# Kernel optimization log

Hardware: AMD Instinct MI355X
Metric: run time of the kernel (lower is better)

## Reference

```python
import jax, jax.numpy as jnp
import numpy as np

N, E, D, H, DH = 10000, 160000, 1024, 4, 256  # nodes, edges, feat dim, heads, per-head dim
NB, G = 3, 64  # num_blocks, num graphs in batch
NEG_SLOPE = 0.2  # PyG GATConv default


def setup_inputs() -> dict:
    key = jax.random.key(0)
    ks = jax.random.split(key, 8)
    x = jax.random.normal(ks[0], (N, D), jnp.float32)
    edge_index = jax.random.randint(ks[1], (2, E), 0, N)
    batch = jnp.sort(jax.random.randint(ks[2], (N,), 0, G))
    W = jax.random.normal(ks[3], (NB, D, H * DH), jnp.float32) * 0.03
    a_src = jax.random.normal(ks[4], (NB, H, DH), jnp.float32) * 0.1
    a_dst = jax.random.normal(ks[5], (NB, H, DH), jnp.float32) * 0.1
    b = jnp.zeros((NB, H * DH), jnp.float32)
    Wr = jax.random.normal(ks[6], (D, 2), jnp.float32) * 0.03
    br = jnp.zeros((2,), jnp.float32)
    return dict(x=x, edge_index=edge_index, batch=batch, W=W, a_src=a_src,
                a_dst=a_dst, b=b, Wr=Wr, br=br)


def _gat_conv(x, src, dst, W, asrc, adst, bias):
    # Linear projection per head: [N, H, DH]
    h = (x @ W).reshape(N, H, DH)
    # Per-node attention logits (src/dst halves of the GAT attention vector)
    es = jnp.einsum('nhd,hd->nh', h, asrc)  # [N, H]
    ed = jnp.einsum('nhd,hd->nh', h, adst)  # [N, H]
    # Edge scores + LeakyReLU
    e = jax.nn.leaky_relu(es[src] + ed[dst], NEG_SLOPE)  # [Etot, H]
    # Segment softmax over edges sharing the same destination node
    m = jax.ops.segment_max(e, dst, num_segments=N)
    p = jnp.exp(e - m[dst])
    s = jax.ops.segment_sum(p, dst, num_segments=N)
    alpha = p / (s[dst] + 1e-16)  # [Etot, H]
    # Scatter-aggregate weighted source features
    out = jax.ops.segment_sum(h[src] * alpha[:, :, None], dst, num_segments=N)
    return out.reshape(N, H * DH) + bias


def reference(x, edge_index, batch, W, a_src, a_dst, b, Wr, br):
    # PyG GATConv adds self-loops by default
    loops = jnp.arange(N)
    src = jnp.concatenate([edge_index[0], loops])
    dst = jnp.concatenate([edge_index[1], loops])
    # Faithful to the source: each block reads the ORIGINAL x; dropout in eval mode.
    h = x
    for i in range(NB):
        h = jax.nn.relu(_gat_conv(x, src, dst, W[i], a_src[i], a_dst[i], b[i]))
    # global_mean_pool over graph assignment `batch`
    sums = jax.ops.segment_sum(h, batch, num_segments=G)
    cnt = jax.ops.segment_sum(jnp.ones((N, 1), h.dtype), batch, num_segments=G)
    pooled = sums / jnp.maximum(cnt, 1.0)
    return pooled @ Wr + br
```

## Files before the change

kernel.cpp:

```cpp
#include <hip/hip_runtime.h>
#include <hip/hip_bf16.h>

#define N_NODES 10000
#define N_EDGES 160000
#define ETOT    (N_NODES + N_EDGES)
#define DIM     1024
#define NHEAD   4
#define DHEAD   256
#define NGRAPH  64
#define NEG_SLOPE 0.2f

typedef short  bf16x8 __attribute__((ext_vector_type(8)));
typedef float  f32x4  __attribute__((ext_vector_type(4)));
typedef unsigned short u16x4 __attribute__((ext_vector_type(4)));
typedef unsigned short u16x8 __attribute__((ext_vector_type(8)));

__device__ __forceinline__ unsigned short f2bf_rne(float v) {
    unsigned u = __builtin_bit_cast(unsigned, v);
    return (unsigned short)((u + 0x7fffu + ((u >> 16) & 1u)) >> 16);
}
__device__ __forceinline__ float bf2f(unsigned short b) {
    return __builtin_bit_cast(float, (unsigned)b << 16);
}
__device__ __forceinline__ float lrelu(float x) { return x > 0.f ? x : NEG_SLOPE * x; }

__global__ __launch_bounds__(256) void prep_x(const float* __restrict__ x,
                                              unsigned short* __restrict__ xhi,
                                              unsigned short* __restrict__ xlo) {
    int i = blockIdx.x * 256 + threadIdx.x;
    if ((size_t)i * 4 >= (size_t)N_NODES * DIM) return;
    f32x4 v = *(const f32x4*)(x + (size_t)i * 4);
    u16x4 hi, lo;
#pragma unroll
    for (int j = 0; j < 4; ++j) {
        unsigned short hb = f2bf_rne(v[j]);
        float r = v[j] - bf2f(hb);
        hi[j] = hb;
        lo[j] = f2bf_rne(r);
    }
    *(u16x4*)(xhi + (size_t)i * 4) = hi;
    *(u16x4*)(xlo + (size_t)i * 4) = lo;
}

__global__ __launch_bounds__(256) void prep_w(const float* __restrict__ W2,
                                              unsigned short* __restrict__ wthi,
                                              unsigned short* __restrict__ wtlo) {
    __shared__ float tile[64][65];
    int bc = blockIdx.x;
    int bk = blockIdx.y;
    int t = threadIdx.x;
    int tj = t & 63, ti = t >> 6;
#pragma unroll
    for (int u = 0; u < 16; ++u) {
        int r = u * 4 + ti;
        tile[r][tj] = W2[(size_t)(bk * 64 + r) * DIM + bc * 64 + tj];
    }
    __syncthreads();
#pragma unroll
    for (int u = 0; u < 16; ++u) {
        int cr = u * 4 + ti;
        float v = tile[tj][cr];
        unsigned short hb = f2bf_rne(v);
        float rres = v - bf2f(hb);
        size_t o = (size_t)(bc * 64 + cr) * DIM + bk * 64 + tj;
        wthi[o] = hb;
        wtlo[o] = f2bf_rne(rres);
    }
}

#define BM 128
#define BN 128
#define BK 32
#define NROWT ((N_NODES + BM - 1) / BM)
#define NCOLT (DIM / BN)

__global__ __launch_bounds__(256) void gemm3(const unsigned short* __restrict__ xhi,
                                             const unsigned short* __restrict__ xlo,
                                             const unsigned short* __restrict__ wthi,
                                             const unsigned short* __restrict__ wtlo,
                                             unsigned short* __restrict__ hb) {
    const int id = blockIdx.x;
    const int xcd = id & 7;
    const int br = xcd + 8 * (id >> 6);
    const int bc = (id >> 3) & 7;
    if (br >= NROWT) return;
    const int r0 = br * BM;
    const int c0 = bc * BN;

    __shared__ short lds[4][BM * BK];
    const int t = threadIdx.x;
    const int lane = t & 63, wid = t >> 6;
    const int wm = wid >> 1, wn = wid & 1;

    const unsigned short* const srcs[4] = {xhi, xlo, wthi, wtlo};
    const unsigned short* wbase = srcs[wid];
    const int rowb = (wid < 2) ? r0 : c0;

    f32x4 acc[4][4];
#pragma unroll
    for (int mi = 0; mi < 4; ++mi)
#pragma unroll
        for (int ni = 0; ni < 4; ++ni) acc[mi][ni] = (f32x4){0.f, 0.f, 0.f, 0.f};

    for (int k0 = 0; k0 < DIM; k0 += BK) {
        __syncthreads();
#pragma unroll
        for (int j = 0; j < 8; ++j) {
            const unsigned short* g = wbase
                + (size_t)(rowb + j * 16 + (lane & 15)) * DIM + k0 + (lane >> 4) * 8;
            __builtin_amdgcn_global_load_lds(
                (const __attribute__((address_space(1))) unsigned int*)g,
                (__attribute__((address_space(3))) unsigned int*)&lds[wid][j * 512],
                16, 0, 0);
        }
        __syncthreads();

        bf16x8 ahi[4], alo[4], bhi[4], blo[4];
#pragma unroll
        for (int mi = 0; mi < 4; ++mi) {
            int sub = wm * 4 + mi;
            ahi[mi] = *(const bf16x8*)&lds[0][sub * 512 + lane * 8];
            alo[mi] = *(const bf16x8*)&lds[1][sub * 512 + lane * 8];
        }
#pragma unroll
        for (int ni = 0; ni < 4; ++ni) {
            int sub = wn * 4 + ni;
            bhi[ni] = *(const bf16x8*)&lds[2][sub * 512 + lane * 8];
            blo[ni] = *(const bf16x8*)&lds[3][sub * 512 + lane * 8];
        }
#pragma unroll
        for (int mi = 0; mi < 4; ++mi)
#pragma unroll
            for (int ni = 0; ni < 4; ++ni) {
                f32x4 c = acc[mi][ni];
                c = __builtin_amdgcn_mfma_f32_16x16x32_bf16(ahi[mi], bhi[ni], c, 0, 0, 0);
                c = __builtin_amdgcn_mfma_f32_16x16x32_bf16(ahi[mi], blo[ni], c, 0, 0, 0);
                c = __builtin_amdgcn_mfma_f32_16x16x32_bf16(alo[mi], bhi[ni], c, 0, 0, 0);
                acc[mi][ni] = c;
            }
    }

#pragma unroll
    for (int mi = 0; mi < 4; ++mi)
#pragma unroll
        for (int ni = 0; ni < 4; ++ni)
#pragma unroll
            for (int v = 0; v < 4; ++v) {
                int row = r0 + wm * 64 + mi * 16 + ((lane >> 4) << 2) + v;
                if (row < N_NODES) {
                    int col = c0 + wn * 64 + ni * 16 + (lane & 15);
                    hb[(size_t)row * DIM + col] = f2bf_rne(acc[mi][ni][v]);
                }
            }
}

__global__ __launch_bounds__(256) void dots_k(const unsigned short* __restrict__ hb,
                                              const float* __restrict__ asrc,
                                              const float* __restrict__ adst,
                                              float* __restrict__ es,
                                              float* __restrict__ ed) {
    int wid = threadIdx.x >> 6, lane = threadIdx.x & 63;
    int n = blockIdx.x * 4 + wid;
    if (n >= N_NODES) return;
    const unsigned short* hr = hb + (size_t)n * DIM + lane * 16;
    u16x8 a = *(const u16x8*)hr;
    u16x8 b8 = *(const u16x8*)(hr + 8);
    const float* ap = asrc + lane * 16;
    const float* dp = adst + lane * 16;
    float sa = 0.f, sd = 0.f;
#pragma unroll
    for (int j = 0; j < 8; ++j) {
        float v = bf2f(a[j]);
        sa += v * ap[j];
        sd += v * dp[j];
    }
#pragma unroll
    for (int j = 0; j < 8; ++j) {
        float v = bf2f(b8[j]);
        sa += v * ap[8 + j];
        sd += v * dp[8 + j];
    }
#pragma unroll
    for (int d = 1; d < 16; d <<= 1) {
        sa += __shfl_xor(sa, d);
        sd += __shfl_xor(sd, d);
    }
    if ((lane & 15) == 0) {
        int head = lane >> 4;
        es[(size_t)n * 4 + head] = sa;
        ed[(size_t)n * 4 + head] = sd;
    }
}

__global__ void init_misc(int* gcnt, int* gbeg, int* gend) {
    int t = threadIdx.x;
    if (t < NGRAPH) { gcnt[t] = 0; gbeg[t] = 0x7fffffff; gend[t] = -1; }
}

__global__ void init_counts(const int* __restrict__ batch, int* cnt, int* cursor,
                            int* gcnt, int* gbeg, int* gend) {
    int n = blockIdx.x * 256 + threadIdx.x;
    if (n >= N_NODES) return;
    cnt[n] = 1;
    cursor[n] = 0;
    int b = batch[n];
    atomicAdd(gcnt + b, 1);
    atomicMin(gbeg + b, n);
    atomicMax(gend + b, n);
}

__global__ void edge_hist(const int* __restrict__ dst, int* cnt) {
    int e = blockIdx.x * 256 + threadIdx.x;
    if (e >= N_EDGES) return;
    atomicAdd(cnt + dst[e], 1);
}

__global__ __launch_bounds__(1024) void scan_k(const int* __restrict__ cnt, int* __restrict__ off) {
    __shared__ int wsh[16];
    __shared__ int tot_s;
    int t = threadIdx.x, lane = t & 63, wv = t >> 6;
    int running = 0;
    for (int c0 = 0; c0 < N_NODES; c0 += 1024) {
        int i = c0 + t;
        int v = (i < N_NODES) ? cnt[i] : 0;
        int s = v;
#pragma unroll
        for (int d = 1; d < 64; d <<= 1) {
            int y = __shfl_up(s, d);
            if (lane >= d) s += y;
        }
        if (lane == 63) wsh[wv] = s;
        __syncthreads();
        if (wv == 0) {
            int wsv = (lane < 16) ? wsh[lane] : 0;
            int e = wsv;
#pragma unroll
            for (int d = 1; d < 16; d <<= 1) {
                int y = __shfl_up(e, d);
                if (lane >= d) e += y;
            }
            if (lane < 16) wsh[lane] = e - wsv;
            if (lane == 15) tot_s = e;
        }
        __syncthreads();
        if (i < N_NODES) off[i] = running + wsh[wv] + s - v;
        running += tot_s;
    }
}

__global__ void bucket_k(const int* __restrict__ src, const int* __restrict__ dst,
                         const int* __restrict__ off, int* cursor, int* bucket) {
    int e = blockIdx.x * 256 + threadIdx.x;
    if (e >= ETOT) return;
    int d = (e < N_EDGES) ? dst[e] : (e - N_EDGES);
    int pos = atomicAdd(cursor + d, 1);
    bucket[off[d] + pos] = e;
}

#define HCAP 192
__global__ __launch_bounds__(256) void aggregate_k(const unsigned short* __restrict__ hb,
                                                   const float* __restrict__ es,
                                                   const float* __restrict__ ed,
                                                   const int* __restrict__ src,
                                                   const int* __restrict__ cnt,
                                                   const int* __restrict__ off,
                                                   const int* __restrict__ bucket,
                                                   const float* __restrict__ b2,
                                                   float* __restrict__ out) {
    int n = blockIdx.x, t = threadIdx.x;
    int deg = cnt[n], base = off[n];
    f32x4 edn = *(const f32x4*)(ed + (size_t)n * 4);
    __shared__ int  s_src[HCAP];
    __shared__ f32x4 s_e[HCAP];
    __shared__ f32x4 wred[4];

    f32x4 m4 = {-3e38f, -3e38f, -3e38f, -3e38f};
    for (int i = t; i < deg; i += 256) {
        int eid = bucket[base + i];
        int s = (eid < N_EDGES) ? src[eid] : (eid - N_EDGES);
        f32x4 e4 = *(const f32x4*)(es + (size_t)s * 4);
        e4.x = lrelu(e4.x + edn.x); e4.y = lrelu(e4.y + edn.y);
        e4.z = lrelu(e4.z + edn.z); e4.w = lrelu(e4.w + edn.w);
        if (i < HCAP) { s_src[i] = s; s_e[i] = e4; }
        m4.x = fmaxf(m4.x, e4.x); m4.y = fmaxf(m4.y, e4.y);
        m4.z = fmaxf(m4.z, e4.z); m4.w = fmaxf(m4.w, e4.w);
    }
#pragma unroll
    for (int d = 1; d < 64; d <<= 1) {
        m4.x = fmaxf(m4.x, __shfl_xor(m4.x, d));
        m4.y = fmaxf(m4.y, __shfl_xor(m4.y, d));
        m4.z = fmaxf(m4.z, __shfl_xor(m4.z, d));
        m4.w = fmaxf(m4.w, __shfl_xor(m4.w, d));
    }
    if ((t & 63) == 0) wred[t >> 6] = m4;
    __syncthreads();
    f32x4 mm = wred[0];
#pragma unroll
    for (int w = 1; w < 4; ++w) {
        mm.x = fmaxf(mm.x, wred[w].x); mm.y = fmaxf(mm.y, wred[w].y);
        mm.z = fmaxf(mm.z, wred[w].z); mm.w = fmaxf(mm.w, wred[w].w);
    }
    int hd = t >> 6;
    float mh = hd == 0 ? mm.x : hd == 1 ? mm.y : hd == 2 ? mm.z : mm.w;

    f32x4 acc = {0.f, 0.f, 0.f, 0.f};
    float sump = 0.f;
    for (int i = 0; i < deg; ++i) {
        int s;
        f32x4 e4;
        if (i < HCAP) { s = s_src[i]; e4 = s_e[i]; }
        else {
            int eid = bucket[base + i];
            s = (eid < N_EDGES) ? src[eid] : (eid - N_EDGES);
            e4 = *(const f32x4*)(es + (size_t)s * 4);
            e4.x = lrelu(e4.x + edn.x); e4.y = lrelu(e4.y + edn.y);
            e4.z = lrelu(e4.z + edn.z); e4.w = lrelu(e4.w + edn.w);
        }
        float eh = hd == 0 ? e4.x : hd == 1 ? e4.y : hd == 2 ? e4.z : e4.w;
        float p = expf(eh - mh);
        sump += p;
        u16x4 q = *(const u16x4*)(hb + (size_t)s * DIM + t * 4);
        f32x4 hv = {bf2f(q[0]), bf2f(q[1]), bf2f(q[2]), bf2f(q[3])};
        acc += p * hv;
    }
    float inv = 1.0f / (sump + 1e-16f);
    f32x4 bb = *(const f32x4*)(b2 + t * 4);
    f32x4 r = acc * inv + bb;
    r.x = fmaxf(r.x, 0.f); r.y = fmaxf(r.y, 0.f);
    r.z = fmaxf(r.z, 0.f); r.w = fmaxf(r.w, 0.f);
    *(f32x4*)(out + (size_t)n * DIM + t * 4) = r;
}

__global__ __launch_bounds__(256) void pool_k(const float* __restrict__ out,
                                              const int* __restrict__ gbeg,
                                              const int* __restrict__ gend,
                                              float* __restrict__ pooled) {
    int g = blockIdx.x, c = blockIdx.y, t = threadIdx.x;
    int col = c * 256 + t;
    int b0 = gbeg[g], b1 = gend[g];
    float acc = 0.f;
    for (int n = b0; n <= b1; ++n) acc += out[(size_t)n * DIM + col];
    pooled[(size_t)g * DIM + col] = acc;
}

__global__ __launch_bounds__(256) void final_k(const float* __restrict__ pooled,
                                               const int* __restrict__ gcnt,
                                               const float* __restrict__ Wr,
                                               const float* __restrict__ br,
                                               float* __restrict__ out) {
    int g = blockIdx.x, t = threadIdx.x;
    float s0 = 0.f, s1 = 0.f;
    for (int d = t; d < DIM; d += 256) {
        float v = pooled[(size_t)g * DIM + d];
        s0 += v * Wr[d * 2];
        s1 += v * Wr[d * 2 + 1];
    }
    __shared__ float r0[256], r1[256];
    r0[t] = s0; r1[t] = s1;
    __syncthreads();
    for (int st = 128; st > 0; st >>= 1) {
        if (t < st) { r0[t] += r0[t + st]; r1[t] += r1[t + st]; }
        __syncthreads();
    }
    if (t == 0) {
        float c = fmaxf((float)gcnt[g], 1.f);
        out[g * 2 + 0] = r0[0] / c + br[0];
        out[g * 2 + 1] = r1[0] / c + br[1];
    }
}

extern "C" void kernel_launch(void* const* d_in, const int* in_sizes, int n_in,
                              void* d_out, int out_size, void* d_ws, size_t ws_size,
                              hipStream_t stream) {
    (void)in_sizes; (void)n_in; (void)out_size; (void)ws_size;
    const float* x     = (const float*)d_in[0];
    const int*   ei    = (const int*)d_in[1];
    const int*   batch = (const int*)d_in[2];
    const float* W     = (const float*)d_in[3];
    const float* a_src = (const float*)d_in[4];
    const float* a_dst = (const float*)d_in[5];
    const float* b     = (const float*)d_in[6];
    const float* Wr    = (const float*)d_in[7];
    const float* br    = (const float*)d_in[8];

    const float* W2    = W + (size_t)2 * DIM * DIM;
    const float* asrc2 = a_src + 2 * NHEAD * DHEAD;
    const float* adst2 = a_dst + 2 * NHEAD * DHEAD;
    const float* b2    = b + 2 * DIM;
    const int* srcI = ei;
    const int* dstI = ei + N_EDGES;

    char* wsp = (char*)d_ws;
    size_t o = 0;
    auto alloc = [&](size_t bytes) -> char* {
        char* p = wsp + o;
        o = (o + bytes + 255) & ~(size_t)255;
        return p;
    };
    unsigned short* xhi  = (unsigned short*)alloc((size_t)N_NODES * DIM * 2);
    unsigned short* xlo  = (unsigned short*)alloc((size_t)N_NODES * DIM * 2);
    unsigned short* wthi = (unsigned short*)alloc((size_t)DIM * DIM * 2);
    unsigned short* wtlo = (unsigned short*)alloc((size_t)DIM * DIM * 2);
    unsigned short* hb   = (unsigned short*)alloc((size_t)N_NODES * DIM * 2);
    float* es   = (float*)alloc((size_t)N_NODES * 4 * 4);
    float* ed   = (float*)alloc((size_t)N_NODES * 4 * 4);
    int*   cnt  = (int*)alloc((size_t)N_NODES * 4);
    int*   offs = (int*)alloc((size_t)N_NODES * 4);
    int*   curs = (int*)alloc((size_t)N_NODES * 4);
    int*   bkt  = (int*)alloc((size_t)ETOT * 4);
    float* pooled = (float*)alloc((size_t)NGRAPH * DIM * 4);
    int*   gcnt   = (int*)alloc(NGRAPH * 4);
    int*   gbeg   = (int*)alloc(NGRAPH * 4);
    int*   gend   = (int*)alloc(NGRAPH * 4);
    float* outn = (float*)xhi;

    init_misc<<<1, 64, 0, stream>>>(gcnt, gbeg, gend);
    prep_x<<<(N_NODES * DIM / 4 + 255) / 256, 256, 0, stream>>>(x, xhi, xlo);
    prep_w<<<dim3(16, 16), 256, 0, stream>>>(W2, wthi, wtlo);
    gemm3<<<((NROWT + 7) / 8) * 8 * NCOLT, 256, 0, stream>>>(xhi, xlo, wthi, wtlo, hb);
    dots_k<<<(N_NODES + 3) / 4, 256, 0, stream>>>(hb, asrc2, adst2, es, ed);

    init_counts<<<(N_NODES + 255) / 256, 256, 0, stream>>>(batch, cnt, curs, gcnt, gbeg, gend);
    edge_hist<<<(N_EDGES + 255) / 256, 256, 0, stream>>>(dstI, cnt);
    scan_k<<<1, 1024, 0, stream>>>(cnt, offs);
    bucket_k<<<(ETOT + 255) / 256, 256, 0, stream>>>(srcI, dstI, offs, curs, bkt);

    aggregate_k<<<N_NODES, 256, 0, stream>>>(hb, es, ed, srcI, cnt, offs, bkt, b2, outn);
    pool_k<<<dim3(NGRAPH, 4), 256, 0, stream>>>(outn, gbeg, gend, pooled);
    final_k<<<NGRAPH, 256, 0, stream>>>(pooled, gcnt, Wr, br, (float*)d_out);
}
```

Before: 440.2 us.

## Pre-tile GEMM operands, fuse attention dots into GEMM epilogue, merge init kernels

prep_x and prep_w now write the bf16 hi/lo operands in a tiled layout that matches the LDS fragment order, so each global_load_lds reads contiguous 1 KB chunks instead of strided rows. The per-node attention dot products move into the GEMM epilogue, using fp32 accumulators with shuffle reductions and atomicAdd into es/ed. This removes the dots_k pass that re-read hb. The init_misc, init_counts and edge_hist kernels are folded into prep_w and a new graph_k, which cuts launch count. The costs are atomics on es/ed, a change from bf16-rounded to fp32 values in the dot products, and zero-init of es/ed that depends on prep_w running first.

```diff
diff --git a/kernel.cpp b/kernel.cpp
--- a/kernel.cpp
+++ b/kernel.cpp
@@ -24,31 +24,52 @@
 }
 __device__ __forceinline__ float lrelu(float x) { return x > 0.f ? x : NEG_SLOPE * x; }
 
+
 __global__ __launch_bounds__(256) void prep_x(const float* __restrict__ x,
                                               unsigned short* __restrict__ xhi,
                                               unsigned short* __restrict__ xlo) {
     int i = blockIdx.x * 256 + threadIdx.x;
-    if ((size_t)i * 4 >= (size_t)N_NODES * DIM) return;
-    f32x4 v = *(const f32x4*)(x + (size_t)i * 4);
-    u16x4 hi, lo;
+    if (i >= N_NODES * 128) return;
+    int row = i >> 7, kseg = i & 127;
+    const float* src = x + (size_t)row * DIM + kseg * 8;
+    f32x4 v0 = *(const f32x4*)src;
+    f32x4 v1 = *(const f32x4*)(src + 4);
+    u16x8 hi, lo;
 #pragma unroll
     for (int j = 0; j < 4; ++j) {
-        unsigned short hb = f2bf_rne(v[j]);
-        float r = v[j] - bf2f(hb);
-        hi[j] = hb;
-        lo[j] = f2bf_rne(r);
-    }
-    *(u16x4*)(xhi + (size_t)i * 4) = hi;
-    *(u16x4*)(xlo + (size_t)i * 4) = lo;
+        unsigned short hb = f2bf_rne(v0[j]);
+        hi[j] = hb; lo[j] = f2bf_rne(v0[j] - bf2f(hb));
+    }
+#pragma unroll
+    for (int j = 0; j < 4; ++j) {
+        unsigned short hb = f2bf_rne(v1[j]);
+        hi[4 + j] = hb; lo[4 + j] = f2bf_rne(v1[j] - bf2f(hb));
+    }
+    size_t off = (size_t)(row >> 4) * 16384 + (kseg >> 2) * 512 + (kseg & 3) * 128 + (row & 15) * 8;
+    *(u16x8*)(xhi + off) = hi;
+    *(u16x8*)(xlo + off) = lo;
 }
 
 __global__ __launch_bounds__(256) void prep_w(const float* __restrict__ W2,
                                               unsigned short* __restrict__ wthi,
-                                              unsigned short* __restrict__ wtlo) {
+                                              unsigned short* __restrict__ wtlo,
+                                              float* __restrict__ es,
+                                              float* __restrict__ ed,
+                                              int* __restrict__ cnt,
+                                              int* __restrict__ curs,
+                                              int* __restrict__ gcnt,
+                                              int* __restrict__ gbeg,
+                                              int* __restrict__ gend) {
     __shared__ float tile[64][65];
     int bc = blockIdx.x;
     int bk = blockIdx.y;
     int t = threadIdx.x;
+
+    int gid = (blockIdx.y * gridDim.x + blockIdx.x) * 256 + t;
+    if (gid < NGRAPH) { gcnt[gid] = 0; gbeg[gid] = 0x7fffffff; gend[gid] = -1; }
+    if (gid < N_NODES) { cnt[gid] = 1; curs[gid] = 0; }
+    if (gid < N_NODES * 4) { es[gid] = 0.f; ed[gid] = 0.f; }
+
     int tj = t & 63, ti = t >> 6;
 #pragma unroll
     for (int u = 0; u < 16; ++u) {
@@ -62,7 +83,10 @@
         float v = tile[tj][cr];
         unsigned short hb = f2bf_rne(v);
         float rres = v - bf2f(hb);
-        size_t o = (size_t)(bc * 64 + cr) * DIM + bk * 64 + tj;
+        int col = bc * 64 + cr;
+        int k = bk * 64 + tj;
+        size_t o = (size_t)(col >> 4) * 16384 + (k >> 5) * 512
+                 + ((k >> 3) & 3) * 128 + (col & 15) * 8 + (k & 7);
         wthi[o] = hb;
         wtlo[o] = f2bf_rne(rres);
     }
@@ -78,7 +102,11 @@
                                              const unsigned short* __restrict__ xlo,
                                              const unsigned short* __restrict__ wthi,
                                              const unsigned short* __restrict__ wtlo,
-                                             unsigned short* __restrict__ hb) {
+                                             const float* __restrict__ asrc,
+                                             const float* __restrict__ adst,
+                                             unsigned short* __restrict__ hb,
+                                             float* __restrict__ es,
+                                             float* __restrict__ ed) {
     const int id = blockIdx.x;
     const int xcd = id & 7;
     const int br = xcd + 8 * (id >> 6);
@@ -93,8 +121,8 @@
     const int wm = wid >> 1, wn = wid & 1;
 
     const unsigned short* const srcs[4] = {xhi, xlo, wthi, wtlo};
-    const unsigned short* wbase = srcs[wid];
-    const int rowb = (wid < 2) ? r0 : c0;
+    const int g0 = ((wid < 2) ? r0 : c0) >> 4;
+    const unsigned short* gsrc = srcs[wid] + (size_t)g0 * 16384 + (size_t)lane * 8;
 
     f32x4 acc[4][4];
 #pragma unroll
@@ -102,12 +130,11 @@
 #pragma unroll
         for (int ni = 0; ni < 4; ++ni) acc[mi][ni] = (f32x4){0.f, 0.f, 0.f, 0.f};
 
-    for (int k0 = 0; k0 < DIM; k0 += BK) {
+    for (int kt = 0; kt < DIM / BK; ++kt) {
         __syncthreads();
 #pragma unroll
         for (int j = 0; j < 8; ++j) {
-            const unsigned short* g = wbase
-                + (size_t)(rowb + j * 16 + (lane & 15)) * DIM + k0 + (lane >> 4) * 8;
+            const unsigned short* g = gsrc + (size_t)j * 16384 + (size_t)kt * 512;
             __builtin_amdgcn_global_load_lds(
                 (const __attribute__((address_space(1))) unsigned int*)g,
                 (__attribute__((address_space(3))) unsigned int*)&lds[wid][j * 512],
@@ -152,67 +179,49 @@
                     hb[(size_t)row * DIM + col] = f2bf_rne(acc[mi][ni][v]);
                 }
             }
-}
-
-__global__ __launch_bounds__(256) void dots_k(const unsigned short* __restrict__ hb,
-                                              const float* __restrict__ asrc,
-                                              const float* __restrict__ adst,
-                                              float* __restrict__ es,
-                                              float* __restrict__ ed) {
-    int wid = threadIdx.x >> 6, lane = threadIdx.x & 63;
-    int n = blockIdx.x * 4 + wid;
-    if (n >= N_NODES) return;
-    const unsigned short* hr = hb + (size_t)n * DIM + lane * 16;
-    u16x8 a = *(const u16x8*)hr;
-    u16x8 b8 = *(const u16x8*)(hr + 8);
-    const float* ap = asrc + lane * 16;
-    const float* dp = adst + lane * 16;
-    float sa = 0.f, sd = 0.f;
-#pragma unroll
-    for (int j = 0; j < 8; ++j) {
-        float v = bf2f(a[j]);
-        sa += v * ap[j];
-        sd += v * dp[j];
-    }
-#pragma unroll
-    for (int j = 0; j < 8; ++j) {
-        float v = bf2f(b8[j]);
-        sa += v * ap[8 + j];
-        sd += v * dp[8 + j];
-    }
-#pragma unroll
-    for (int d = 1; d < 16; d <<= 1) {
-        sa += __shfl_xor(sa, d);
-        sd += __shfl_xor(sd, d);
-    }
-    if ((lane & 15) == 0) {
-        int head = lane >> 4;
-        es[(size_t)n * 4 + head] = sa;
-        ed[(size_t)n * 4 + head] = sd;
-    }
-}
-
-__global__ void init_misc(int* gcnt, int* gbeg, int* gend) {
-    int t = threadIdx.x;
-    if (t < NGRAPH) { gcnt[t] = 0; gbeg[t] = 0x7fffffff; gend[t] = -1; }
-}
-
-__global__ void init_counts(const int* __restrict__ batch, int* cnt, int* cursor,
-                            int* gcnt, int* gbeg, int* gend) {
-    int n = blockIdx.x * 256 + threadIdx.x;
-    if (n >= N_NODES) return;
-    cnt[n] = 1;
-    cursor[n] = 0;
-    int b = batch[n];
-    atomicAdd(gcnt + b, 1);
-    atomicMin(gbeg + b, n);
-    atomicMax(gend + b, n);
-}
-
-__global__ void edge_hist(const int* __restrict__ dst, int* cnt) {
+
+    const int head = c0 >> 8;
+    float as_c[4], ad_c[4];
+#pragma unroll
+    for (int ni = 0; ni < 4; ++ni) {
+        int col = c0 + wn * 64 + ni * 16 + (lane & 15);
+        as_c[ni] = asrc[col];
+        ad_c[ni] = adst[col];
+    }
+#pragma unroll
+    for (int mi = 0; mi < 4; ++mi)
+#pragma unroll
+        for (int v = 0; v < 4; ++v) {
+            float pe = 0.f, pd = 0.f;
+#pragma unroll
+            for (int ni = 0; ni < 4; ++ni) {
+                float a = acc[mi][ni][v];
+                pe += a * as_c[ni];
+                pd += a * ad_c[ni];
+            }
+#pragma unroll
+            for (int d = 1; d < 16; d <<= 1) {
+                pe += __shfl_xor(pe, d);
+                pd += __shfl_xor(pd, d);
+            }
+            int row = r0 + wm * 64 + mi * 16 + ((lane >> 4) << 2) + v;
+            if ((lane & 15) == 0 && row < N_NODES) {
+                atomicAdd(es + row * 4 + head, pe);
+                atomicAdd(ed + row * 4 + head, pd);
+            }
+        }
+}
+
+__global__ void graph_k(const int* __restrict__ dst, const int* __restrict__ batch,
+                        int* cnt, int* gcnt, int* gbeg, int* gend) {
     int e = blockIdx.x * 256 + threadIdx.x;
-    if (e >= N_EDGES) return;
-    atomicAdd(cnt + dst[e], 1);
+    if (e < N_EDGES) atomicAdd(cnt + dst[e], 1);
+    if (e < N_NODES) {
+        int b = batch[e];
+        atomicAdd(gcnt + b, 1);
+        atomicMin(gbeg + b, e);
+        atomicMax(gend + b, e);
+    }
 }
 
 __global__ __launch_bounds__(1024) void scan_k(const int* __restrict__ cnt, int* __restrict__ off) {
@@ -414,14 +423,11 @@
     int*   gend   = (int*)alloc(NGRAPH * 4);
     float* outn = (float*)xhi;
 
-    init_misc<<<1, 64, 0, stream>>>(gcnt, gbeg, gend);
-    prep_x<<<(N_NODES * DIM / 4 + 255) / 256, 256, 0, stream>>>(x, xhi, xlo);
-    prep_w<<<dim3(16, 16), 256, 0, stream>>>(W2, wthi, wtlo);
-    gemm3<<<((NROWT + 7) / 8) * 8 * NCOLT, 256, 0, stream>>>(xhi, xlo, wthi, wtlo, hb);
-    dots_k<<<(N_NODES + 3) / 4, 256, 0, stream>>>(hb, asrc2, adst2, es, ed);
-
-    init_counts<<<(N_NODES + 255) / 256, 256, 0, stream>>>(batch, cnt, curs, gcnt, gbeg, gend);
-    edge_hist<<<(N_EDGES + 255) / 256, 256, 0, stream>>>(dstI, cnt);
+    prep_x<<<(N_NODES * 128 + 255) / 256, 256, 0, stream>>>(x, xhi, xlo);
+    prep_w<<<dim3(16, 16), 256, 0, stream>>>(W2, wthi, wtlo, es, ed, cnt, curs, gcnt, gbeg, gend);
+    gemm3<<<((NROWT + 7) / 8) * 8 * NCOLT, 256, 0, stream>>>(xhi, xlo, wthi, wtlo,
+                                                             asrc2, adst2, hb, es, ed);
+    graph_k<<<(N_EDGES + 255) / 256, 256, 0, stream>>>(dstI, batch, cnt, gcnt, gbeg, gend);
     scan_k<<<1, 1024, 0, stream>>>(cnt, offs);
     bucket_k<<<(ETOT + 255) / 256, 256, 0, stream>>>(srcI, dstI, offs, curs, bkt);
 
```

After: 422.8 us. 1.04x faster.
